# Optimization experiments

Measured on AMD Instinct MI355X. Metric: run time of the kernel, lower is better.

Reference implementation:

```python
import jax, jax.numpy as jnp
import numpy as np

B, P, ENC = 64, 196, 512
E, H, A, V, L = 1024, 1024, 512, 20000, 25


def setup_inputs() -> dict:
    key = jax.random.key(0)
    ks = jax.random.split(key, 20)
    s = 0.02
    return {
        "encoder_out": jax.random.normal(ks[0], (B, P, ENC), jnp.float32),
        "captions": jax.random.randint(ks[1], (B, L), 0, V),
        "lengths": L,
        # attention MLP
        "W_enc_att": jax.random.normal(ks[2], (ENC, A), jnp.float32) * s,
        "b_enc_att": jnp.zeros((A,), jnp.float32),
        "W_dec_att": jax.random.normal(ks[3], (H, A), jnp.float32) * s,
        "b_dec_att": jnp.zeros((A,), jnp.float32),
        "W_full_att": jax.random.normal(ks[4], (A, 1), jnp.float32) * s,
        "b_full_att": jnp.zeros((1,), jnp.float32),
        # embedding
        "emb_table": jax.random.normal(ks[5], (V, E), jnp.float32) * s,
        # LSTMCell: input = embedding + context -> (E+ENC, 4H)
        "W_ih": jax.random.normal(ks[6], (E + ENC, 4 * H), jnp.float32) * s,
        "b_ih": jnp.zeros((4 * H,), jnp.float32),
        "W_hh": jax.random.normal(ks[7], (H, 4 * H), jnp.float32) * s,
        "b_hh": jnp.zeros((4 * H,), jnp.float32),
        # init states
        "W_init_h": jax.random.normal(ks[8], (ENC, H), jnp.float32) * s,
        "b_init_h": jnp.zeros((H,), jnp.float32),
        "W_init_c": jax.random.normal(ks[9], (ENC, H), jnp.float32) * s,
        "b_init_c": jnp.zeros((H,), jnp.float32),
        # gate + output proj
        "W_fbeta": jax.random.normal(ks[10], (H, ENC), jnp.float32) * s,
        "b_fbeta": jnp.zeros((ENC,), jnp.float32),
        "W_fc": jax.random.normal(ks[11], (H, V), jnp.float32) * s,
        "b_fc": jnp.zeros((V,), jnp.float32),
    }


def _decode(encoder_out, W_enc_att, b_enc_att, W_dec_att, b_dec_att,
            W_full_att, b_full_att, emb_table, W_ih, b_ih, W_hh, b_hh,
            W_init_h, b_init_h, W_init_c, b_init_c, W_fbeta, b_fbeta,
            W_fc, b_fc, captions, T):
    # precompute encoder-side attention projection (constant across timesteps)
    att_enc = encoder_out @ W_enc_att + b_enc_att          # (B, P, A)
    mean_feat = encoder_out.mean(axis=1)                   # (B, ENC)
    h0 = mean_feat @ W_init_h + b_init_h
    c0 = mean_feat @ W_init_c + b_init_c
    embeddings = emb_table[captions[:, :T]]                # (B, T, E)
    xs = jnp.swapaxes(embeddings, 0, 1)                    # (T, B, E)

    def step(carry, emb_t):
        h, c = carry
        att_dec = h @ W_dec_att + b_dec_att                # (B, A)
        energy = (jax.nn.relu(att_enc + att_dec[:, None, :]) @ W_full_att
                  + b_full_att)[..., 0]                    # (B, P)
        alpha = jax.nn.softmax(energy, axis=1)
        context = jnp.einsum('bp,bpe->be', alpha, encoder_out)
        gate = jax.nn.sigmoid(h @ W_fbeta + b_fbeta)       # (B, ENC)
        x = jnp.concatenate([emb_t, gate * context], axis=1)
        gates = x @ W_ih + b_ih + h @ W_hh + b_hh          # (B, 4H)
        i, f, g, o = jnp.split(gates, 4, axis=1)           # torch order i,f,g,o
        c = jax.nn.sigmoid(f) * c + jax.nn.sigmoid(i) * jnp.tanh(g)
        h = jax.nn.sigmoid(o) * jnp.tanh(c)
        preds = h @ W_fc + b_fc                            # dropout = identity (eval)
        return (h, c), (preds, alpha)

    _, (preds, alphas) = jax.lax.scan(step, (h0, c0), xs)
    predictions = jnp.swapaxes(preds, 0, 1)                # (B, T, V)
    alphas = jnp.swapaxes(alphas, 0, 1)                    # (B, T, P)
    return predictions, alphas


def reference(encoder_out, captions, lengths, W_enc_att, b_enc_att, W_dec_att,
              b_dec_att, W_full_att, b_full_att, emb_table, W_ih, b_ih, W_hh,
              b_hh, W_init_h, b_init_h, W_init_c, b_init_c, W_fbeta, b_fbeta,
              W_fc, b_fc):
    T = int(lengths) - 1
    return _decode(encoder_out, W_enc_att, b_enc_att, W_dec_att, b_dec_att,
                   W_full_att, b_full_att, emb_table, W_ih, b_ih, W_hh, b_hh,
                   W_init_h, b_init_h, W_init_c, b_init_c, W_fbeta, b_fbeta,
                   W_fc, b_fc, captions, T)
```

## Files before the change

### kernel.cpp

```cpp
#include <hip/hip_runtime.h>
#include <hip/hip_bf16.h>

#define BB 64
#define PP 196
#define ENCD 512
#define ED 1024
#define HD 1024
#define AD 512
#define VD 20000
#define TT 24
#define VPAD 20096
#define HOFF 32768
#define NSA 4

typedef __attribute__((ext_vector_type(8))) short short8;
typedef __attribute__((ext_vector_type(4))) short short4v;
typedef __attribute__((ext_vector_type(4))) float f32x4;
typedef __attribute__((ext_vector_type(8))) _Float16 h16x8;

__device__ __forceinline__ float sigf(float x) { return 1.f / (1.f + __expf(-x)); }

__device__ __forceinline__ unsigned short f2bf(float f) {
    unsigned u = __builtin_bit_cast(unsigned, f);
    u = (u + 0x7FFFu + ((u >> 16) & 1u)) >> 16;
    return (unsigned short)u;
}
__device__ __forceinline__ void split2(float v, unsigned short& h, unsigned short& l) {
    h = f2bf(v);
    float hf = __builtin_bit_cast(float, ((unsigned)h) << 16);
    l = f2bf(v - hf);
}
__device__ __forceinline__ void split2h(float v, _Float16& h, _Float16& l) {
    h = (_Float16)v;
    l = (_Float16)(v - (float)h);
}
__device__ __forceinline__ float bf2f(unsigned short u) {
    return __builtin_bit_cast(float, ((unsigned)u) << 16);
}

__device__ __forceinline__ void split_store(
    const float* __restrict__ W, unsigned short* __restrict__ oh,
    unsigned short* __restrict__ ol, int N, int Npad, int coff,
    int rowoff, int perm, int kc, int n) {
    int src = perm ? ((n & 3) * 1024 + (n >> 2)) : n;
    short8 vh, vl;
    #pragma unroll
    for (int j = 0; j < 8; ++j) {
        float v = (src < N) ? W[(size_t)(rowoff + kc * 8 + j) * N + src] : 0.f;
        unsigned short h, l; split2(v, h, l);
        vh[j] = (short)h; vl[j] = (short)l;
    }
    size_t o = ((size_t)kc * Npad + coff + n) * 8;
    *(short8*)(oh + o) = vh; *(short8*)(ol + o) = vl;
}

__global__ __launch_bounds__(256) void megasplit_kernel(
    const float* __restrict__ W_enc, unsigned short* __restrict__ wenc_h, unsigned short* __restrict__ wenc_l,
    const float* __restrict__ W_dec, const float* __restrict__ W_fbeta, const float* __restrict__ W_hh,
    unsigned short* __restrict__ wbig_h, unsigned short* __restrict__ wbig_l,
    const float* __restrict__ W_ih,
    unsigned short* __restrict__ wih1_h, unsigned short* __restrict__ wih1_l,
    unsigned short* __restrict__ wih2_h, unsigned short* __restrict__ wih2_l,
    const float* __restrict__ b_ih, const float* __restrict__ b_hh, float* __restrict__ biasp,
    const int* __restrict__ captions, const float* __restrict__ table,
    unsigned short* __restrict__ embc_h, unsigned short* __restrict__ embc_l) {
    int bid = blockIdx.x, tid = threadIdx.x;
    if (bid < 128) {
        int local = bid, xb = local & 1, kc = local >> 1;
        split_store(W_enc, wenc_h, wenc_l, 512, 512, 0, 0, 0, kc, xb * 256 + tid);
    } else if (bid < 384) {
        int local = bid - 128, xb = local & 1, kc = local >> 1;
        split_store(W_dec, wbig_h, wbig_l, 512, 5120, 0, 0, 0, kc, xb * 256 + tid);
    } else if (bid < 640) {
        int local = bid - 384, xb = local & 1, kc = local >> 1;
        split_store(W_fbeta, wbig_h, wbig_l, 512, 5120, 512, 0, 0, kc, xb * 256 + tid);
    } else if (bid < 2688) {
        int local = bid - 640, xb = local & 15, kc = local >> 4;
        split_store(W_hh, wbig_h, wbig_l, 4096, 5120, 1024, 0, 1, kc, xb * 256 + tid);
    } else if (bid < 4736) {
        int local = bid - 2688, xb = local & 15, kc = local >> 4;
        split_store(W_ih, wih1_h, wih1_l, 4096, 4096, 0, 0, 1, kc, xb * 256 + tid);
    } else if (bid < 5760) {
        int local = bid - 4736, xb = local & 15, kc = local >> 4;
        split_store(W_ih, wih2_h, wih2_l, 4096, 4096, 0, 1024, 1, kc, xb * 256 + tid);
    } else if (bid < 5776) {
        int n = (bid - 5760) * 256 + tid;
        int src = (n & 3) * 1024 + (n >> 2);
        biasp[n] = b_ih[src] + b_hh[src];
    } else {
        int local = bid - 5776;
        int t = local >> 6, b = local & 63;
        if (tid < 128) {
            int kc = tid;
            int tok = captions[b * 25 + t];
            const float* row = table + (size_t)tok * ED + kc * 8;
            short8 vh, vl;
            #pragma unroll
            for (int j = 0; j < 8; ++j) {
                unsigned short h, l; split2(row[j], h, l);
                vh[j] = (short)h; vl[j] = (short)l;
            }
            size_t o = ((size_t)kc * (TT * BB) + t * BB + b) * 8;
            *(short8*)(embc_h + o) = vh; *(short8*)(embc_l + o) = vl;
        }
    }
}

__global__ __launch_bounds__(256) void enc2bf16_kernel(
    const float* __restrict__ enc, unsigned short* __restrict__ encb) {
    size_t idx = ((size_t)blockIdx.x * 256 + threadIdx.x) * 8;
    float4 v0 = *(const float4*)(enc + idx);
    float4 v1 = *(const float4*)(enc + idx + 4);
    short8 o;
    o[0] = (short)f2bf(v0.x); o[1] = (short)f2bf(v0.y);
    o[2] = (short)f2bf(v0.z); o[3] = (short)f2bf(v0.w);
    o[4] = (short)f2bf(v1.x); o[5] = (short)f2bf(v1.y);
    o[6] = (short)f2bf(v1.z); o[7] = (short)f2bf(v1.w);
    *(short8*)(encb + idx) = o;
}

__global__ __launch_bounds__(256) void split_w_fp16_kernel(
    const float* __restrict__ W, _Float16* __restrict__ oq,
    int N, int Npad, int Nlaunch) {
    int n = blockIdx.x * 256 + threadIdx.x;
    if (n >= Nlaunch) return;
    int kc = blockIdx.y;
    h16x8 v;
    #pragma unroll
    for (int j = 0; j < 8; ++j)
        v[j] = (_Float16)((n < N) ? W[(size_t)(kc * 8 + j) * N + n] : 0.f);
    *(h16x8*)(oq + ((size_t)kc * Npad + n) * 8) = v;
}

__global__ __launch_bounds__(512) void mean_kernel(const float* __restrict__ enc,
                                                   float* __restrict__ mf) {
    int b = blockIdx.x; int e = threadIdx.x;
    const float* base = enc + (size_t)b * PP * ENCD + e;
    float s = 0.f;
    #pragma unroll 4
    for (int p = 0; p < PP; ++p) s += base[(size_t)p * ENCD];
    mf[b * ENCD + e] = s * (1.f / PP);
}

__global__ __launch_bounds__(256) void init_hc_kernel(
    const float* __restrict__ mf,
    const float* __restrict__ Wh, const float* __restrict__ bh,
    const float* __restrict__ Wc, const float* __restrict__ bc,
    unsigned short* __restrict__ hc_h, unsigned short* __restrict__ hc_l,
    float* __restrict__ c0) {
    int b = blockIdx.x;
    int isC = blockIdx.y;
    const float* W    = isC ? Wc : Wh;
    const float* bias = isC ? bc : bh;
    __shared__ float smf[ENCD];
    for (int i = threadIdx.x; i < ENCD; i += 256) smf[i] = mf[b * ENCD + i];
    __syncthreads();
    #pragma unroll
    for (int jj = 0; jj < 4; ++jj) {
        int j = threadIdx.x + jj * 256;
        float acc = bias[j];
        for (int k = 0; k < ENCD; ++k) acc += smf[k] * W[(size_t)k * HD + j];
        if (isC) c0[b * HD + j] = acc;
        else {
            unsigned short h, l; split2(acc, h, l);
            size_t o = ((size_t)(j >> 3) * 64 + b) * 8 + (j & 7);
            hc_h[o] = h; hc_l[o] = l;
        }
    }
}

__global__ __launch_bounds__(256) void mfma_gemm_bigf(
    const float* __restrict__ Ap,
    const unsigned short* __restrict__ Bh, const unsigned short* __restrict__ Bl,
    const float* __restrict__ bias, float* __restrict__ C,
    int N, int Npad, int K, int Mtiles, int Ntiles, int inner_m, int half_out) {
    __shared__ __align__(16) short lds[32768];
    short* Ahs = lds;
    short* Als = lds + 8192;
    short* Bhs = lds + 16384;
    short* Bls = lds + 24576;
    int tid = threadIdx.x, lane = tid & 63, w = tid >> 6;
    int nwg = Mtiles * Ntiles;
    int orig = blockIdx.x;
    int q = nwg >> 3, r = nwg & 7;
    int xcd = orig & 7;
    int basew = (xcd < r) ? xcd * (q + 1) : r * (q + 1) + (xcd - r) * q;
    int wg = basew + (orig >> 3);
    int mt, nt;
    if (inner_m) { mt = wg % Mtiles; nt = wg / Mtiles; }
    else         { nt = wg % Ntiles; mt = wg / Ntiles; }
    int m0 = mt * 128, n0 = nt * 128;
    int wr = w >> 1, wc = w & 1;
    f32x4 acc[4][4];
    #pragma unroll
    for (int i = 0; i < 4; ++i)
        #pragma unroll
        for (int j = 0; j < 4; ++j) acc[i][j] = (f32x4){0.f, 0.f, 0.f, 0.f};
    int nsteps = K >> 6;
    float4 va[8];
    short8 rb[2][4];
    auto load_step = [&](int s) {
        int k0 = s * 64, kc0 = s * 8;
        #pragma unroll
        for (int it = 0; it < 8; ++it) {
            int idx = it * 256 + tid; int m = idx >> 4, k4 = idx & 15;
            va[it] = *(const float4*)(Ap + (size_t)(m0 + m) * K + k0 + k4 * 4);
        }
        #pragma unroll
        for (int it = 0; it < 4; ++it) {
            int g = w * 4 + it; int kcl = g >> 1; int rb0 = (g & 1) * 64;
            size_t gb = ((size_t)(kc0 + kcl) * Npad + n0 + rb0 + lane) * 8;
            rb[0][it] = *(const short8*)(Bh + gb);
            rb[1][it] = *(const short8*)(Bl + gb);
        }
    };
    load_step(0);
    for (int s = 0; s < nsteps; ++s) {
        __syncthreads();
        #pragma unroll
        for (int it = 0; it < 8; ++it) {
            int idx = it * 256 + tid; int m = idx >> 4, k4 = idx & 15;
            int kc = k4 >> 1, jh = (k4 & 1) * 4;
            float vv[4] = {va[it].x, va[it].y, va[it].z, va[it].w};
            short4v hv, lv;
            #pragma unroll
            for (int qq = 0; qq < 4; ++qq) {
                unsigned short h, l; split2(vv[qq], h, l);
                hv[qq] = (short)h; lv[qq] = (short)l;
            }
            int o = kc * 1024 + ((m ^ kc) << 3) + jh;
            *(short4v*)(Ahs + o) = hv;
            *(short4v*)(Als + o) = lv;
        }
        #pragma unroll
        for (int it = 0; it < 4; ++it) {
            int g = w * 4 + it; int kcl = g >> 1; int rb0 = (g & 1) * 64;
            int o = (kcl * 128 + rb0 + lane) * 8;
            *(short8*)(Bhs + o) = rb[0][it];
            *(short8*)(Bls + o) = rb[1][it];
        }
        __syncthreads();
        if (s + 1 < nsteps) load_step(s + 1);
        #pragma unroll
        for (int ks = 0; ks < 2; ++ks) {
            int kq = ks * 4 + (lane >> 4);
            short8 afh[4], afl[4], bfh[4], bfl[4];
            #pragma unroll
            for (int mi = 0; mi < 4; ++mi) {
                int row = wr * 64 + mi * 16 + (lane & 15);
                int o = kq * 1024 + ((row ^ kq) << 3);
                afh[mi] = *(const short8*)(Ahs + o);
                afl[mi] = *(const short8*)(Als + o);
            }
            #pragma unroll
            for (int ni = 0; ni < 4; ++ni) {
                int o = (kq * 128 + wc * 64 + ni * 16 + (lane & 15)) * 8;
                bfh[ni] = *(const short8*)(Bhs + o);
                bfl[ni] = *(const short8*)(Bls + o);
            }
            #pragma unroll
            for (int mi = 0; mi < 4; ++mi)
                #pragma unroll
                for (int ni = 0; ni < 4; ++ni) {
                    acc[mi][ni] = __builtin_amdgcn_mfma_f32_16x16x32_bf16(afh[mi], bfh[ni], acc[mi][ni], 0, 0, 0);
                    acc[mi][ni] = __builtin_amdgcn_mfma_f32_16x16x32_bf16(afh[mi], bfl[ni], acc[mi][ni], 0, 0, 0);
                    acc[mi][ni] = __builtin_amdgcn_mfma_f32_16x16x32_bf16(afl[mi], bfh[ni], acc[mi][ni], 0, 0, 0);
                }
        }
    }
    #pragma unroll
    for (int mi = 0; mi < 4; ++mi) {
        int rrow = m0 + wr * 64 + mi * 16 + ((lane >> 4) << 2);
        #pragma unroll
        for (int ni = 0; ni < 4; ++ni) {
            int c = n0 + wc * 64 + ni * 16 + (lane & 15);
            if (c < N) {
                float bv = bias ? bias[c] : 0.f;
                if (half_out) {
                    _Float16* Ch = (_Float16*)C;
                    #pragma unroll
                    for (int qq = 0; qq < 4; ++qq)
                        Ch[(size_t)(rrow + qq) * N + c] = (_Float16)(acc[mi][ni][qq] + bv);
                } else {
                    #pragma unroll
                    for (int qq = 0; qq < 4; ++qq)
                        C[(size_t)(rrow + qq) * N + c] = acc[mi][ni][qq] + bv;
                }
            }
        }
    }
}

__global__ __launch_bounds__(256) void mfma_gemm_bigp(
    const unsigned short* __restrict__ Ah, const unsigned short* __restrict__ Al,
    const unsigned short* __restrict__ Bh, const unsigned short* __restrict__ Bl,
    const float* __restrict__ bias, float* __restrict__ C,
    int Mtot, int N, int Npad, int K, int Mtiles, int Ntiles, int inner_m) {
    __shared__ __align__(16) short lds[32768];
    short* Ahs = lds;
    short* Als = lds + 8192;
    short* Bhs = lds + 16384;
    short* Bls = lds + 24576;
    int tid = threadIdx.x, lane = tid & 63, w = tid >> 6;
    int nwg = Mtiles * Ntiles;
    int orig = blockIdx.x;
    int q = nwg >> 3, r = nwg & 7;
    int xcd = orig & 7;
    int basew = (xcd < r) ? xcd * (q + 1) : r * (q + 1) + (xcd - r) * q;
    int wg = basew + (orig >> 3);
    int mt, nt;
    if (inner_m) { mt = wg % Mtiles; nt = wg / Mtiles; }
    else         { nt = wg % Ntiles; mt = wg / Ntiles; }
    int m0 = mt * 128, n0 = nt * 128;
    int wr = w >> 1, wc = w & 1;
    f32x4 acc[4][4];
    #pragma unroll
    for (int i = 0; i < 4; ++i)
        #pragma unroll
        for (int j = 0; j < 4; ++j) acc[i][j] = (f32x4){0.f, 0.f, 0.f, 0.f};
    int nsteps = K >> 6;
    short8 ra[2][4], rb[2][4];
    auto load_step = [&](int s) {
        int kc0 = s * 8;
        #pragma unroll
        for (int it = 0; it < 4; ++it) {
            int idx = it * 256 + tid; int kcl = idx >> 7, row = idx & 127;
            size_t ga = ((size_t)(kc0 + kcl) * Mtot + m0 + row) * 8;
            ra[0][it] = *(const short8*)(Ah + ga);
            ra[1][it] = *(const short8*)(Al + ga);
        }
        #pragma unroll
        for (int it = 0; it < 4; ++it) {
            int g = w * 4 + it; int kcl = g >> 1; int rb0 = (g & 1) * 64;
            size_t gb = ((size_t)(kc0 + kcl) * Npad + n0 + rb0 + lane) * 8;
            rb[0][it] = *(const short8*)(Bh + gb);
            rb[1][it] = *(const short8*)(Bl + gb);
        }
    };
    load_step(0);
    for (int s = 0; s < nsteps; ++s) {
        __syncthreads();
        #pragma unroll
        for (int it = 0; it < 4; ++it) {
            int idx = it * 256 + tid; int kcl = idx >> 7, row = idx & 127;
            int o = (kcl * 128 + row) * 8;
            *(short8*)(Ahs + o) = ra[0][it];
            *(short8*)(Als + o) = ra[1][it];
        }
        #pragma unroll
        for (int it = 0; it < 4; ++it) {
            int g = w * 4 + it; int kcl = g >> 1; int rb0 = (g & 1) * 64;
            int o = (kcl * 128 + rb0 + lane) * 8;
            *(short8*)(Bhs + o) = rb[0][it];
            *(short8*)(Bls + o) = rb[1][it];
        }
        __syncthreads();
        if (s + 1 < nsteps) load_step(s + 1);
        #pragma unroll
        for (int ks = 0; ks < 2; ++ks) {
            int kq = ks * 4 + (lane >> 4);
            short8 afh[4], afl[4], bfh[4], bfl[4];
            #pragma unroll
            for (int mi = 0; mi < 4; ++mi) {
                int o = (kq * 128 + wr * 64 + mi * 16 + (lane & 15)) * 8;
                afh[mi] = *(const short8*)(Ahs + o);
                afl[mi] = *(const short8*)(Als + o);
            }
            #pragma unroll
            for (int ni = 0; ni < 4; ++ni) {
                int o = (kq * 128 + wc * 64 + ni * 16 + (lane & 15)) * 8;
                bfh[ni] = *(const short8*)(Bhs + o);
                bfl[ni] = *(const short8*)(Bls + o);
            }
            #pragma unroll
            for (int mi = 0; mi < 4; ++mi)
                #pragma unroll
                for (int ni = 0; ni < 4; ++ni) {
                    acc[mi][ni] = __builtin_amdgcn_mfma_f32_16x16x32_bf16(afh[mi], bfh[ni], acc[mi][ni], 0, 0, 0);
                    acc[mi][ni] = __builtin_amdgcn_mfma_f32_16x16x32_bf16(afh[mi], bfl[ni], acc[mi][ni], 0, 0, 0);
                    acc[mi][ni] = __builtin_amdgcn_mfma_f32_16x16x32_bf16(afl[mi], bfh[ni], acc[mi][ni], 0, 0, 0);
                }
        }
    }
    #pragma unroll
    for (int mi = 0; mi < 4; ++mi) {
        int rrow = m0 + wr * 64 + mi * 16 + ((lane >> 4) << 2);
        #pragma unroll
        for (int ni = 0; ni < 4; ++ni) {
            int c = n0 + wc * 64 + ni * 16 + (lane & 15);
            if (c < N) {
                float bv = bias ? bias[c] : 0.f;
                #pragma unroll
                for (int qq = 0; qq < 4; ++qq)
                    C[(size_t)(rrow + qq) * N + c] = acc[mi][ni][qq] + bv;
            }
        }
    }
}

__global__ __launch_bounds__(256) void mfma_gemm_fp16(
    const _Float16* __restrict__ Ah, const _Float16* __restrict__ Al,
    const _Float16* __restrict__ Bq,
    const float* __restrict__ bias, float* __restrict__ C,
    int Mtot, int N, int Npad, int K, int Mtiles, int Ntiles) {
    __shared__ __align__(16) _Float16 lds[24576];
    _Float16* Ahs = lds;
    _Float16* Als = lds + 8192;
    _Float16* Bs  = lds + 16384;
    int tid = threadIdx.x, lane = tid & 63, w = tid >> 6;
    int nwg = Mtiles * Ntiles;
    int orig = blockIdx.x;
    int q = nwg >> 3, r = nwg & 7;
    int xcd = orig & 7;
    int basew = (xcd < r) ? xcd * (q + 1) : r * (q + 1) + (xcd - r) * q;
    int wg = basew + (orig >> 3);
    int mt = wg % Mtiles, nt = wg / Mtiles;
    int m0 = mt * 128, n0 = nt * 128;
    int wr = w >> 1, wc = w & 1;
    f32x4 acc[4][4];
    #pragma unroll
    for (int i = 0; i < 4; ++i)
        #pragma unroll
        for (int j = 0; j < 4; ++j) acc[i][j] = (f32x4){0.f, 0.f, 0.f, 0.f};
    int nsteps = K >> 6;
    h16x8 ra[2][4], rb[4];
    auto load_step = [&](int s) {
        int kc0 = s * 8;
        #pragma unroll
        for (int it = 0; it < 4; ++it) {
            int idx = it * 256 + tid; int kcl = idx >> 7, row = idx & 127;
            size_t ga = ((size_t)(kc0 + kcl) * Mtot + m0 + row) * 8;
            ra[0][it] = *(const h16x8*)(Ah + ga);
            ra[1][it] = *(const h16x8*)(Al + ga);
        }
        #pragma unroll
        for (int it = 0; it < 4; ++it) {
            int idx = it * 256 + tid; int kcl = idx >> 7, row = idx & 127;
            size_t gb = ((size_t)(kc0 + kcl) * Npad + n0 + row) * 8;
            rb[it] = *(const h16x8*)(Bq + gb);
        }
    };
    load_step(0);
    for (int s = 0; s < nsteps; ++s) {
        __syncthreads();
        #pragma unroll
        for (int it = 0; it < 4; ++it) {
            int idx = it * 256 + tid; int kcl = idx >> 7, row = idx & 127;
            int o = (kcl * 128 + row) * 8;
            *(h16x8*)(Ahs + o) = ra[0][it];
            *(h16x8*)(Als + o) = ra[1][it];
            *(h16x8*)(Bs + o)  = rb[it];
        }
        __syncthreads();
        if (s + 1 < nsteps) load_step(s + 1);
        #pragma unroll
        for (int ks = 0; ks < 2; ++ks) {
            int kq = ks * 4 + (lane >> 4);
            h16x8 afh[4], afl[4], bf[4];
            #pragma unroll
            for (int mi = 0; mi < 4; ++mi) {
                int o = (kq * 128 + wr * 64 + mi * 16 + (lane & 15)) * 8;
                afh[mi] = *(const h16x8*)(Ahs + o);
                afl[mi] = *(const h16x8*)(Als + o);
            }
            #pragma unroll
            for (int ni = 0; ni < 4; ++ni) {
                int o = (kq * 128 + wc * 64 + ni * 16 + (lane & 15)) * 8;
                bf[ni] = *(const h16x8*)(Bs + o);
            }
            #pragma unroll
            for (int mi = 0; mi < 4; ++mi)
                #pragma unroll
                for (int ni = 0; ni < 4; ++ni) {
                    acc[mi][ni] = __builtin_amdgcn_mfma_f32_16x16x32_f16(afh[mi], bf[ni], acc[mi][ni], 0, 0, 0);
                    acc[mi][ni] = __builtin_amdgcn_mfma_f32_16x16x32_f16(afl[mi], bf[ni], acc[mi][ni], 0, 0, 0);
                }
        }
    }
    #pragma unroll
    for (int mi = 0; mi < 4; ++mi) {
        int rrow = m0 + wr * 64 + mi * 16 + ((lane >> 4) << 2);
        #pragma unroll
        for (int ni = 0; ni < 4; ++ni) {
            int c = n0 + wc * 64 + ni * 16 + (lane & 15);
            if (c < N) {
                float bv = bias ? bias[c] : 0.f;
                #pragma unroll
                for (int qq = 0; qq < 4; ++qq)
                    C[(size_t)(rrow + qq) * N + c] = acc[mi][ni][qq] + bv;
            }
        }
    }
}

__global__ __launch_bounds__(256) void hgemm_direct(
    const unsigned short* __restrict__ Ah, const unsigned short* __restrict__ Al,
    const unsigned short* __restrict__ Bh, const unsigned short* __restrict__ Bl,
    float* __restrict__ out) {
    int tid = threadIdx.x, lane = tid & 63, w = tid >> 6;
    int n0 = blockIdx.x * 128 + w * 32;
    int kc0 = blockIdx.y * 32;
    out += (size_t)blockIdx.y * 64 * 5120;
    f32x4 acc[4][2];
    #pragma unroll
    for (int i = 0; i < 4; ++i)
        #pragma unroll
        for (int j = 0; j < 2; ++j) acc[i][j] = (f32x4){0.f, 0.f, 0.f, 0.f};
    #pragma unroll
    for (int s = 0; s < 8; ++s) {
        int kc = kc0 + s * 4 + (lane >> 4);
        short8 afh[4], afl[4], bfh[2], bfl[2];
        #pragma unroll
        for (int mi = 0; mi < 4; ++mi) {
            size_t o = ((size_t)kc * 64 + mi * 16 + (lane & 15)) * 8;
            afh[mi] = *(const short8*)(Ah + o);
            afl[mi] = *(const short8*)(Al + o);
        }
        #pragma unroll
        for (int ni = 0; ni < 2; ++ni) {
            size_t o = ((size_t)kc * 5120 + n0 + ni * 16 + (lane & 15)) * 8;
            bfh[ni] = *(const short8*)(Bh + o);
            bfl[ni] = *(const short8*)(Bl + o);
        }
        #pragma unroll
        for (int mi = 0; mi < 4; ++mi)
            #pragma unroll
            for (int ni = 0; ni < 2; ++ni) {
                acc[mi][ni] = __builtin_amdgcn_mfma_f32_16x16x32_bf16(afh[mi], bfh[ni], acc[mi][ni], 0, 0, 0);
                acc[mi][ni] = __builtin_amdgcn_mfma_f32_16x16x32_bf16(afh[mi], bfl[ni], acc[mi][ni], 0, 0, 0);
                acc[mi][ni] = __builtin_amdgcn_mfma_f32_16x16x32_bf16(afl[mi], bfh[ni], acc[mi][ni], 0, 0, 0);
            }
    }
    #pragma unroll
    for (int mi = 0; mi < 4; ++mi) {
        int rrow = mi * 16 + ((lane >> 4) << 2);
        #pragma unroll
        for (int ni = 0; ni < 2; ++ni) {
            int c = n0 + ni * 16 + (lane & 15);
            #pragma unroll
            for (int qq = 0; qq < 4; ++qq)
                out[(size_t)(rrow + qq) * 5120 + c] = acc[mi][ni][qq];
        }
    }
}

__global__ __launch_bounds__(1024) void attn_ctx_kernel(
    const _Float16* __restrict__ att_enc, const float* __restrict__ adg,
    const float* __restrict__ b_dec, const float* __restrict__ Wfull,
    const unsigned short* __restrict__ encb, const float* __restrict__ b_fbeta,
    float* __restrict__ alpha_out, unsigned short* __restrict__ x2h,
    unsigned short* __restrict__ x2l, int t) {
    int b = blockIdx.x; int tid = threadIdx.x;
    __shared__ float sdec[AD], sw[AD], sgate[AD], sal[256], sE[256], red[256];
    __shared__ float sctx[2][AD];
    if (tid < AD) {
        float s = b_dec[tid];
        #pragma unroll
        for (int ks = 0; ks < NSA; ++ks) s += adg[((size_t)ks * BB + b) * 5120 + tid];
        sdec[tid] = s;
        sw[tid] = Wfull[tid];
    } else {
        int e = tid - AD;
        float s = b_fbeta[e];
        #pragma unroll
        for (int ks = 0; ks < NSA; ++ks) s += adg[((size_t)ks * BB + b) * 5120 + 512 + e];
        sgate[e] = s;
    }
    __syncthreads();
    int w = tid >> 6, lane = tid & 63;
    float4 sd0 = *(const float4*)&sdec[lane * 8];
    float4 sd1 = *(const float4*)&sdec[lane * 8 + 4];
    float4 sw0 = *(const float4*)&sw[lane * 8];
    float4 sw1 = *(const float4*)&sw[lane * 8 + 4];
    for (int p = w; p < PP; p += 16) {
        const _Float16* row = att_enc + ((size_t)b * PP + p) * AD + lane * 8;
        h16x8 hv = *(const h16x8*)row;
        float part = fmaxf((float)hv[0] + sd0.x, 0.f) * sw0.x +
                     fmaxf((float)hv[1] + sd0.y, 0.f) * sw0.y +
                     fmaxf((float)hv[2] + sd0.z, 0.f) * sw0.z +
                     fmaxf((float)hv[3] + sd0.w, 0.f) * sw0.w +
                     fmaxf((float)hv[4] + sd1.x, 0.f) * sw1.x +
                     fmaxf((float)hv[5] + sd1.y, 0.f) * sw1.y +
                     fmaxf((float)hv[6] + sd1.z, 0.f) * sw1.z +
                     fmaxf((float)hv[7] + sd1.w, 0.f) * sw1.w;
        #pragma unroll
        for (int off = 32; off > 0; off >>= 1) part += __shfl_down(part, off, 64);
        if (lane == 0) sE[p] = part;
    }
    __syncthreads();
    float myE = (tid < PP) ? sE[tid] : -1e30f;
    if (tid < 256) red[tid] = myE;
    __syncthreads();
    for (int s = 128; s > 0; s >>= 1) {
        if (tid < s) red[tid] = fmaxf(red[tid], red[tid + s]);
        __syncthreads();
    }
    float mx = red[0];
    __syncthreads();
    float ex = (tid < PP) ? __expf(myE - mx) : 0.f;
    if (tid < 256) red[tid] = ex;
    __syncthreads();
    for (int s = 128; s > 0; s >>= 1) {
        if (tid < s) red[tid] += red[tid + s];
        __syncthreads();
    }
    if (tid < PP) {
        float al = ex * (1.f / red[0]);
        sal[tid] = al;
        alpha_out[((size_t)b * TT + t) * PP + tid] = al;
    }
    __syncthreads();
    int e = tid & 511, half = tid >> 9;
    const unsigned short* basep = encb + (size_t)b * PP * ENCD + e;
    float s2 = 0.f;
    #pragma unroll 2
    for (int p = half * 98; p < half * 98 + 98; ++p)
        s2 += sal[p] * bf2f(basep[(size_t)p * ENCD]);
    sctx[half][e] = s2;
    __syncthreads();
    if (tid < AD) {
        float ctx = sctx[0][tid] + sctx[1][tid];
        float gate = sigf(sgate[tid]);
        unsigned short h, l; split2(gate * ctx, h, l);
        size_t o = ((size_t)(tid >> 3) * 64 + b) * 8 + (tid & 7);
        x2h[o] = h; x2l[o] = l;
    }
}

__global__ __launch_bounds__(256) void gates_lstm2(
    const unsigned short* __restrict__ Ah, const unsigned short* __restrict__ Al,
    const unsigned short* __restrict__ Bh, const unsigned short* __restrict__ Bl,
    const float* __restrict__ pregates, const float* __restrict__ adg,
    float* __restrict__ c, unsigned short* __restrict__ ho_h,
    unsigned short* __restrict__ ho_l, _Float16* __restrict__ hfc_h,
    _Float16* __restrict__ hfc_l, int t) {
    __shared__ float gl[4][64][33];
    int tid = threadIdx.x, lane = tid & 63, w = tid >> 6;
    int n0 = blockIdx.x * 32;
    f32x4 acc[4][2];
    #pragma unroll
    for (int i = 0; i < 4; ++i)
        #pragma unroll
        for (int j = 0; j < 2; ++j) acc[i][j] = (f32x4){0.f, 0.f, 0.f, 0.f};
    #pragma unroll
    for (int s = 0; s < 4; ++s) {
        int kc = w * 16 + s * 4 + (lane >> 4);
        short8 afh[4], afl[4], bfh[2], bfl[2];
        #pragma unroll
        for (int mi = 0; mi < 4; ++mi) {
            size_t o = ((size_t)kc * 64 + mi * 16 + (lane & 15)) * 8;
            afh[mi] = *(const short8*)(Ah + o);
            afl[mi] = *(const short8*)(Al + o);
        }
        #pragma unroll
        for (int ni = 0; ni < 2; ++ni) {
            size_t o = ((size_t)kc * 4096 + n0 + ni * 16 + (lane & 15)) * 8;
            bfh[ni] = *(const short8*)(Bh + o);
            bfl[ni] = *(const short8*)(Bl + o);
        }
        #pragma unroll
        for (int mi = 0; mi < 4; ++mi)
            #pragma unroll
            for (int ni = 0; ni < 2; ++ni) {
                acc[mi][ni] = __builtin_amdgcn_mfma_f32_16x16x32_bf16(afh[mi], bfh[ni], acc[mi][ni], 0, 0, 0);
                acc[mi][ni] = __builtin_amdgcn_mfma_f32_16x16x32_bf16(afh[mi], bfl[ni], acc[mi][ni], 0, 0, 0);
                acc[mi][ni] = __builtin_amdgcn_mfma_f32_16x16x32_bf16(afl[mi], bfh[ni], acc[mi][ni], 0, 0, 0);
            }
    }
    #pragma unroll
    for (int mi = 0; mi < 4; ++mi) {
        int rrow = mi * 16 + ((lane >> 4) << 2);
        #pragma unroll
        for (int ni = 0; ni < 2; ++ni) {
            int cl = ni * 16 + (lane & 15);
            #pragma unroll
            for (int qq = 0; qq < 4; ++qq)
                gl[w][rrow + qq][cl] = acc[mi][ni][qq];
        }
    }
    __syncthreads();
    #pragma unroll
    for (int i = 0; i < 2; ++i) {
        int idx = tid + i * 256;
        int b = idx >> 3, jl = idx & 7;
        float g4[4];
        #pragma unroll
        for (int qq = 0; qq < 4; ++qq)
            g4[qq] = gl[0][b][4 * jl + qq] + gl[1][b][4 * jl + qq] +
                     gl[2][b][4 * jl + qq] + gl[3][b][4 * jl + qq];
        {
            float4 pv = *(const float4*)&pregates[((size_t)(t * 64 + b)) * 4096 + n0 + 4 * jl];
            g4[0] += pv.x; g4[1] += pv.y; g4[2] += pv.z; g4[3] += pv.w;
        }
        #pragma unroll
        for (int ks = 0; ks < NSA; ++ks) {
            float4 av = *(const float4*)&adg[((size_t)ks * BB + b) * 5120 + 1024 + n0 + 4 * jl];
            g4[0] += av.x; g4[1] += av.y; g4[2] += av.z; g4[3] += av.w;
        }
        int j = (n0 >> 2) + jl;
        float cn = sigf(g4[1]) * c[b * HD + j] + sigf(g4[0]) * tanhf(g4[2]);
        c[b * HD + j] = cn;
        float hn = sigf(g4[3]) * tanhf(cn);
        unsigned short h, l; split2(hn, h, l);
        size_t o1 = ((size_t)(j >> 3) * 64 + b) * 8 + (j & 7);
        ho_h[o1] = h; ho_l[o1] = l;
        _Float16 fh, fl; split2h(hn, fh, fl);
        size_t o2 = ((size_t)(j >> 3) * (TT * BB) + b * TT + t) * 8 + (j & 7);
        hfc_h[o2] = fh; hfc_l[o2] = fl;
    }
}

extern "C" void kernel_launch(void* const* d_in, const int* in_sizes, int n_in,
                              void* d_out, int out_size, void* d_ws, size_t ws_size,
                              hipStream_t stream) {
    const float* enc      = (const float*)d_in[0];
    const int*   captions = (const int*)d_in[1];
    const float* W_enc    = (const float*)d_in[3];
    const float* b_enc    = (const float*)d_in[4];
    const float* W_dec    = (const float*)d_in[5];
    const float* b_dec    = (const float*)d_in[6];
    const float* W_full   = (const float*)d_in[7];
    const float* table    = (const float*)d_in[9];
    const float* W_ih     = (const float*)d_in[10];
    const float* b_ih     = (const float*)d_in[11];
    const float* W_hh     = (const float*)d_in[12];
    const float* b_hh     = (const float*)d_in[13];
    const float* W_init_h = (const float*)d_in[14];
    const float* b_init_h = (const float*)d_in[15];
    const float* W_init_c = (const float*)d_in[16];
    const float* b_init_c = (const float*)d_in[17];
    const float* W_fbeta  = (const float*)d_in[18];
    const float* b_fbeta  = (const float*)d_in[19];
    const float* W_fc     = (const float*)d_in[20];
    const float* b_fc     = (const float*)d_in[21];

    float* preds  = (float*)d_out;
    float* alphas = (float*)d_out + (size_t)BB * TT * VD;

    char* base = (char*)d_ws;
    size_t off = 0;
    auto take = [&](size_t b) { void* r = (void*)(base + off); off += (b + 255) & ~(size_t)255; return r; };
    _Float16* att_enc = (_Float16*)take((size_t)12544 * 512 * 2);
    unsigned short* wbig_h = (unsigned short*)take((size_t)128 * 5120 * 8 * 2);
    unsigned short* wbig_l = (unsigned short*)take((size_t)128 * 5120 * 8 * 2);
    unsigned short* wih1_h = (unsigned short*)take((size_t)128 * 4096 * 8 * 2);
    unsigned short* wih1_l = (unsigned short*)take((size_t)128 * 4096 * 8 * 2);
    unsigned short* encb   = (unsigned short*)wih1_h;
    unsigned short* wih2_h = (unsigned short*)take((size_t)64 * 4096 * 8 * 2);
    unsigned short* wih2_l = (unsigned short*)take((size_t)64 * 4096 * 8 * 2);
    unsigned short* wenc_h = (unsigned short*)take((size_t)64 * 512 * 8 * 2);
    unsigned short* wenc_l = (unsigned short*)take((size_t)64 * 512 * 8 * 2);
    float* pregates = (float*)take((size_t)TT * BB * 4096 * 4);
    float* scratch0 = (float*)take((size_t)TT * BB * ED * 4);
    unsigned short* embc_h = (unsigned short*)scratch0;
    unsigned short* embc_l = embc_h + (size_t)128 * TT * BB * 8;
    float* adg      = scratch0;
    float* biasp    = (float*)take((size_t)4096 * 4);
    _Float16* wfc_q = (_Float16*)(base);
    float* c_buf = (float*)take((size_t)BB * HD * 4);
    float* mf    = (float*)take((size_t)BB * ENCD * 4);
    unsigned short* axh_h0 = (unsigned short*)take((size_t)192 * 64 * 8 * 2);
    unsigned short* axh_l0 = (unsigned short*)take((size_t)192 * 64 * 8 * 2);
    unsigned short* axh_h1 = (unsigned short*)take((size_t)192 * 64 * 8 * 2);
    unsigned short* axh_l1 = (unsigned short*)take((size_t)192 * 64 * 8 * 2);
    _Float16* hfc_h  = (_Float16*)take((size_t)128 * TT * BB * 8 * 2);
    _Float16* hfc_l  = (_Float16*)take((size_t)128 * TT * BB * 8 * 2);

    megasplit_kernel<<<7312, 256, 0, stream>>>(
        W_enc, wenc_h, wenc_l, W_dec, W_fbeta, W_hh, wbig_h, wbig_l,
        W_ih, wih1_h, wih1_l, wih2_h, wih2_l,
        b_ih, b_hh, biasp, captions, table, embc_h, embc_l);
    mean_kernel<<<BB, 512, 0, stream>>>(enc, mf);
    init_hc_kernel<<<dim3(BB, 2), 256, 0, stream>>>(mf, W_init_h, b_init_h, W_init_c, b_init_c,
                                                    axh_h0 + HOFF, axh_l0 + HOFF, c_buf);
    mfma_gemm_bigf<<<392, 256, 0, stream>>>(enc, wenc_h, wenc_l, b_enc, (float*)att_enc,
                                            512, 512, 512, 98, 4, 0, 1);
    mfma_gemm_bigp<<<384, 256, 0, stream>>>(embc_h, embc_l, wih1_h, wih1_l, biasp, pregates,
                                            TT * BB, 4096, 4096, 1024, 12, 32, 1);
    enc2bf16_kernel<<<3136, 256, 0, stream>>>(enc, encb);

    {
        unsigned short* ah[2] = {axh_h0, axh_h1};
        unsigned short* al[2] = {axh_l0, axh_l1};
        for (int t = 0; t < TT; ++t) {
            int par = t & 1;
            hgemm_direct<<<dim3(40, NSA), 256, 0, stream>>>(
                ah[par] + HOFF, al[par] + HOFF, wbig_h, wbig_l, adg);
            attn_ctx_kernel<<<BB, 1024, 0, stream>>>(att_enc, adg, b_dec, W_full, encb,
                                                     b_fbeta, alphas, ah[par], al[par], t);
            gates_lstm2<<<128, 256, 0, stream>>>(
                ah[par], al[par], wih2_h, wih2_l, pregates, adg, c_buf,
                ah[1 - par] + HOFF, al[1 - par] + HOFF, hfc_h, hfc_l, t);
        }
    }

    split_w_fp16_kernel<<<dim3(79, 128), 256, 0, stream>>>(W_fc, wfc_q, VD, VPAD, VPAD);
    mfma_gemm_fp16<<<1884, 256, 0, stream>>>(hfc_h, hfc_l, wfc_q, b_fc, preds,
                                             TT * BB, VD, VPAD, 1024, 12, 157);
}
```

Baseline: 1.471 ms.

## Fuse decoder attention projection into attention kernel and W_hh into gates GEMM

Removes the per-step split-bf16 MFMA GEMM over W_dec/W_fbeta/W_hh. The attention kernel now computes the decoder projection and f_beta gate itself, using a scalar fp32 dot product per block against a concatenated 1024x1024 weight. The W_hh term moves into the gates GEMM by lengthening its K dimension from 512 to 1536. This drops one kernel launch per timestep and the adg round trip. In exchange, each of the 64 attention blocks re-reads the full 4MB fp32 weight matrix with scalar FMAs, and the gates kernel does three times more K work in only 128 blocks.

```diff
diff --git a/kernel.cpp b/kernel.cpp
--- a/kernel.cpp
+++ b/kernel.cpp
@@ -11,7 +11,6 @@
 #define TT 24
 #define VPAD 20096
 #define HOFF 32768
-#define NSA 4
 
 typedef __attribute__((ext_vector_type(8))) short short8;
 typedef __attribute__((ext_vector_type(4))) short short4v;
@@ -56,11 +55,10 @@
 
 __global__ __launch_bounds__(256) void megasplit_kernel(
     const float* __restrict__ W_enc, unsigned short* __restrict__ wenc_h, unsigned short* __restrict__ wenc_l,
-    const float* __restrict__ W_dec, const float* __restrict__ W_fbeta, const float* __restrict__ W_hh,
-    unsigned short* __restrict__ wbig_h, unsigned short* __restrict__ wbig_l,
-    const float* __restrict__ W_ih,
+    const float* __restrict__ W_dec, const float* __restrict__ W_fbeta, float* __restrict__ wdecfb,
+    const float* __restrict__ W_ih, const float* __restrict__ W_hh,
     unsigned short* __restrict__ wih1_h, unsigned short* __restrict__ wih1_l,
-    unsigned short* __restrict__ wih2_h, unsigned short* __restrict__ wih2_l,
+    unsigned short* __restrict__ wg2_h, unsigned short* __restrict__ wg2_l,
     const float* __restrict__ b_ih, const float* __restrict__ b_hh, float* __restrict__ biasp,
     const int* __restrict__ captions, const float* __restrict__ table,
     unsigned short* __restrict__ embc_h, unsigned short* __restrict__ embc_l) {
@@ -68,27 +66,26 @@
     if (bid < 128) {
         int local = bid, xb = local & 1, kc = local >> 1;
         split_store(W_enc, wenc_h, wenc_l, 512, 512, 0, 0, 0, kc, xb * 256 + tid);
-    } else if (bid < 384) {
-        int local = bid - 128, xb = local & 1, kc = local >> 1;
-        split_store(W_dec, wbig_h, wbig_l, 512, 5120, 0, 0, 0, kc, xb * 256 + tid);
-    } else if (bid < 640) {
-        int local = bid - 384, xb = local & 1, kc = local >> 1;
-        split_store(W_fbeta, wbig_h, wbig_l, 512, 5120, 512, 0, 0, kc, xb * 256 + tid);
-    } else if (bid < 2688) {
-        int local = bid - 640, xb = local & 15, kc = local >> 4;
-        split_store(W_hh, wbig_h, wbig_l, 4096, 5120, 1024, 0, 1, kc, xb * 256 + tid);
-    } else if (bid < 4736) {
-        int local = bid - 2688, xb = local & 15, kc = local >> 4;
+    } else if (bid < 4224) {
+        int idx = (bid - 128) * 256 + tid;
+        int k = idx >> 10, n = idx & 1023;
+        wdecfb[idx] = (n < 512) ? W_dec[(size_t)k * 512 + n] : W_fbeta[(size_t)k * 512 + (n - 512)];
+    } else if (bid < 6272) {
+        int local = bid - 4224, xb = local & 15, kc = local >> 4;
         split_store(W_ih, wih1_h, wih1_l, 4096, 4096, 0, 0, 1, kc, xb * 256 + tid);
-    } else if (bid < 5760) {
-        int local = bid - 4736, xb = local & 15, kc = local >> 4;
-        split_store(W_ih, wih2_h, wih2_l, 4096, 4096, 0, 1024, 1, kc, xb * 256 + tid);
-    } else if (bid < 5776) {
-        int n = (bid - 5760) * 256 + tid;
+    } else if (bid < 7296) {
+        int local = bid - 6272, xb = local & 15, kc = local >> 4;
+        split_store(W_ih, wg2_h, wg2_l, 4096, 4096, 0, 1024, 1, kc, xb * 256 + tid);
+    } else if (bid < 9344) {
+        int local = bid - 7296, xb = local & 15, kc = local >> 4;
+        split_store(W_hh, wg2_h + (size_t)64 * 4096 * 8, wg2_l + (size_t)64 * 4096 * 8,
+                    4096, 4096, 0, 0, 1, kc, xb * 256 + tid);
+    } else if (bid < 9360) {
+        int n = (bid - 9344) * 256 + tid;
         int src = (n & 3) * 1024 + (n >> 2);
         biasp[n] = b_ih[src] + b_hh[src];
     } else {
-        int local = bid - 5776;
+        int local = bid - 9360;
         int t = local >> 6, b = local & 63;
         if (tid < 128) {
             int kc = tid;
@@ -493,78 +490,39 @@
     }
 }
 
-__global__ __launch_bounds__(256) void hgemm_direct(
-    const unsigned short* __restrict__ Ah, const unsigned short* __restrict__ Al,
-    const unsigned short* __restrict__ Bh, const unsigned short* __restrict__ Bl,
-    float* __restrict__ out) {
-    int tid = threadIdx.x, lane = tid & 63, w = tid >> 6;
-    int n0 = blockIdx.x * 128 + w * 32;
-    int kc0 = blockIdx.y * 32;
-    out += (size_t)blockIdx.y * 64 * 5120;
-    f32x4 acc[4][2];
-    #pragma unroll
-    for (int i = 0; i < 4; ++i)
-        #pragma unroll
-        for (int j = 0; j < 2; ++j) acc[i][j] = (f32x4){0.f, 0.f, 0.f, 0.f};
-    #pragma unroll
-    for (int s = 0; s < 8; ++s) {
-        int kc = kc0 + s * 4 + (lane >> 4);
-        short8 afh[4], afl[4], bfh[2], bfl[2];
-        #pragma unroll
-        for (int mi = 0; mi < 4; ++mi) {
-            size_t o = ((size_t)kc * 64 + mi * 16 + (lane & 15)) * 8;
-            afh[mi] = *(const short8*)(Ah + o);
-            afl[mi] = *(const short8*)(Al + o);
-        }
-        #pragma unroll
-        for (int ni = 0; ni < 2; ++ni) {
-            size_t o = ((size_t)kc * 5120 + n0 + ni * 16 + (lane & 15)) * 8;
-            bfh[ni] = *(const short8*)(Bh + o);
-            bfl[ni] = *(const short8*)(Bl + o);
-        }
-        #pragma unroll
-        for (int mi = 0; mi < 4; ++mi)
-            #pragma unroll
-            for (int ni = 0; ni < 2; ++ni) {
-                acc[mi][ni] = __builtin_amdgcn_mfma_f32_16x16x32_bf16(afh[mi], bfh[ni], acc[mi][ni], 0, 0, 0);
-                acc[mi][ni] = __builtin_amdgcn_mfma_f32_16x16x32_bf16(afh[mi], bfl[ni], acc[mi][ni], 0, 0, 0);
-                acc[mi][ni] = __builtin_amdgcn_mfma_f32_16x16x32_bf16(afl[mi], bfh[ni], acc[mi][ni], 0, 0, 0);
-            }
-    }
-    #pragma unroll
-    for (int mi = 0; mi < 4; ++mi) {
-        int rrow = mi * 16 + ((lane >> 4) << 2);
-        #pragma unroll
-        for (int ni = 0; ni < 2; ++ni) {
-            int c = n0 + ni * 16 + (lane & 15);
-            #pragma unroll
-            for (int qq = 0; qq < 4; ++qq)
-                out[(size_t)(rrow + qq) * 5120 + c] = acc[mi][ni][qq];
-        }
-    }
-}
-
-__global__ __launch_bounds__(1024) void attn_ctx_kernel(
-    const _Float16* __restrict__ att_enc, const float* __restrict__ adg,
-    const float* __restrict__ b_dec, const float* __restrict__ Wfull,
-    const unsigned short* __restrict__ encb, const float* __restrict__ b_fbeta,
+__global__ __launch_bounds__(1024) void attn2_kernel(
+    const unsigned short* __restrict__ hh, const unsigned short* __restrict__ hl,
+    const float* __restrict__ wdecfb, const float* __restrict__ b_dec,
+    const float* __restrict__ b_fbeta, const float* __restrict__ Wfull,
+    const _Float16* __restrict__ att_enc, const unsigned short* __restrict__ encb,
     float* __restrict__ alpha_out, unsigned short* __restrict__ x2h,
     unsigned short* __restrict__ x2l, int t) {
     int b = blockIdx.x; int tid = threadIdx.x;
-    __shared__ float sdec[AD], sw[AD], sgate[AD], sal[256], sE[256], red[256];
+    __shared__ float shh[1024], sdec[AD], sgate[AD], sw[AD], sal[256], sE[256], red[256];
     __shared__ float sctx[2][AD];
-    if (tid < AD) {
-        float s = b_dec[tid];
-        #pragma unroll
-        for (int ks = 0; ks < NSA; ++ks) s += adg[((size_t)ks * BB + b) * 5120 + tid];
-        sdec[tid] = s;
-        sw[tid] = Wfull[tid];
-    } else {
-        int e = tid - AD;
-        float s = b_fbeta[e];
-        #pragma unroll
-        for (int ks = 0; ks < NSA; ++ks) s += adg[((size_t)ks * BB + b) * 5120 + 512 + e];
-        sgate[e] = s;
+    if (tid < 128) {
+        short8 vh = *(const short8*)(hh + ((size_t)tid * 64 + b) * 8);
+        short8 vl = *(const short8*)(hl + ((size_t)tid * 64 + b) * 8);
+        #pragma unroll
+        for (int j = 0; j < 8; ++j)
+            shh[tid * 8 + j] = bf2f((unsigned short)vh[j]) + bf2f((unsigned short)vl[j]);
+    }
+    if (tid < AD) sw[tid] = Wfull[tid];
+    __syncthreads();
+    {
+        int n = tid;
+        float a0 = 0.f, a1 = 0.f, a2 = 0.f, a3 = 0.f;
+        const float* wp = wdecfb + n;
+        #pragma unroll 4
+        for (int k = 0; k < 1024; k += 4) {
+            a0 += shh[k]     * wp[(size_t)k * 1024];
+            a1 += shh[k + 1] * wp[(size_t)(k + 1) * 1024];
+            a2 += shh[k + 2] * wp[(size_t)(k + 2) * 1024];
+            a3 += shh[k + 3] * wp[(size_t)(k + 3) * 1024];
+        }
+        float acc = (a0 + a1) + (a2 + a3);
+        if (n < AD) sdec[n] = acc + b_dec[n];
+        else        sgate[n - AD] = acc + b_fbeta[n - AD];
     }
     __syncthreads();
     int w = tid >> 6, lane = tid & 63;
@@ -627,13 +585,12 @@
     }
 }
 
-__global__ __launch_bounds__(256) void gates_lstm2(
+__global__ __launch_bounds__(256) void gates2_kernel(
     const unsigned short* __restrict__ Ah, const unsigned short* __restrict__ Al,
     const unsigned short* __restrict__ Bh, const unsigned short* __restrict__ Bl,
-    const float* __restrict__ pregates, const float* __restrict__ adg,
-    float* __restrict__ c, unsigned short* __restrict__ ho_h,
-    unsigned short* __restrict__ ho_l, _Float16* __restrict__ hfc_h,
-    _Float16* __restrict__ hfc_l, int t) {
+    const float* __restrict__ pregates, float* __restrict__ c,
+    unsigned short* __restrict__ ho_h, unsigned short* __restrict__ ho_l,
+    _Float16* __restrict__ hfc_h, _Float16* __restrict__ hfc_l, int t) {
     __shared__ float gl[4][64][33];
     int tid = threadIdx.x, lane = tid & 63, w = tid >> 6;
     int n0 = blockIdx.x * 32;
@@ -643,8 +600,8 @@
         #pragma unroll
         for (int j = 0; j < 2; ++j) acc[i][j] = (f32x4){0.f, 0.f, 0.f, 0.f};
     #pragma unroll
-    for (int s = 0; s < 4; ++s) {
-        int kc = w * 16 + s * 4 + (lane >> 4);
+    for (int s = 0; s < 12; ++s) {
+        int kc = w * 48 + s * 4 + (lane >> 4);
         short8 afh[4], afl[4], bfh[2], bfl[2];
         #pragma unroll
         for (int mi = 0; mi < 4; ++mi) {
@@ -691,11 +648,6 @@
         {
             float4 pv = *(const float4*)&pregates[((size_t)(t * 64 + b)) * 4096 + n0 + 4 * jl];
             g4[0] += pv.x; g4[1] += pv.y; g4[2] += pv.z; g4[3] += pv.w;
-        }
-        #pragma unroll
-        for (int ks = 0; ks < NSA; ++ks) {
-            float4 av = *(const float4*)&adg[((size_t)ks * BB + b) * 5120 + 1024 + n0 + 4 * jl];
-            g4[0] += av.x; g4[1] += av.y; g4[2] += av.z; g4[3] += av.w;
         }
         int j = (n0 >> 2) + jl;
         float cn = sigf(g4[1]) * c[b * HD + j] + sigf(g4[0]) * tanhf(g4[2]);
@@ -741,20 +693,17 @@
     size_t off = 0;
     auto take = [&](size_t b) { void* r = (void*)(base + off); off += (b + 255) & ~(size_t)255; return r; };
     _Float16* att_enc = (_Float16*)take((size_t)12544 * 512 * 2);
-    unsigned short* wbig_h = (unsigned short*)take((size_t)128 * 5120 * 8 * 2);
-    unsigned short* wbig_l = (unsigned short*)take((size_t)128 * 5120 * 8 * 2);
+    unsigned short* wg2_h  = (unsigned short*)take((size_t)192 * 4096 * 8 * 2);
+    unsigned short* wg2_l  = (unsigned short*)take((size_t)192 * 4096 * 8 * 2);
     unsigned short* wih1_h = (unsigned short*)take((size_t)128 * 4096 * 8 * 2);
     unsigned short* wih1_l = (unsigned short*)take((size_t)128 * 4096 * 8 * 2);
     unsigned short* encb   = (unsigned short*)wih1_h;
-    unsigned short* wih2_h = (unsigned short*)take((size_t)64 * 4096 * 8 * 2);
-    unsigned short* wih2_l = (unsigned short*)take((size_t)64 * 4096 * 8 * 2);
+    float* wdecfb = (float*)take((size_t)1024 * 1024 * 4);
     unsigned short* wenc_h = (unsigned short*)take((size_t)64 * 512 * 8 * 2);
     unsigned short* wenc_l = (unsigned short*)take((size_t)64 * 512 * 8 * 2);
     float* pregates = (float*)take((size_t)TT * BB * 4096 * 4);
-    float* scratch0 = (float*)take((size_t)TT * BB * ED * 4);
-    unsigned short* embc_h = (unsigned short*)scratch0;
-    unsigned short* embc_l = embc_h + (size_t)128 * TT * BB * 8;
-    float* adg      = scratch0;
+    unsigned short* embc_h = (unsigned short*)take((size_t)128 * TT * BB * 8 * 2);
+    unsigned short* embc_l = (unsigned short*)take((size_t)128 * TT * BB * 8 * 2);
     float* biasp    = (float*)take((size_t)4096 * 4);
     _Float16* wfc_q = (_Float16*)(base);
     float* c_buf = (float*)take((size_t)BB * HD * 4);
@@ -766,10 +715,10 @@
     _Float16* hfc_h  = (_Float16*)take((size_t)128 * TT * BB * 8 * 2);
     _Float16* hfc_l  = (_Float16*)take((size_t)128 * TT * BB * 8 * 2);
 
-    megasplit_kernel<<<7312, 256, 0, stream>>>(
-        W_enc, wenc_h, wenc_l, W_dec, W_fbeta, W_hh, wbig_h, wbig_l,
-        W_ih, wih1_h, wih1_l, wih2_h, wih2_l,
-        b_ih, b_hh, biasp, captions, table, embc_h, embc_l);
+    megasplit_kernel<<<10896, 256, 0, stream>>>(
+        W_enc, wenc_h, wenc_l, W_dec, W_fbeta, wdecfb, W_ih, W_hh,
+        wih1_h, wih1_l, wg2_h, wg2_l, b_ih, b_hh, biasp,
+        captions, table, embc_h, embc_l);
     mean_kernel<<<BB, 512, 0, stream>>>(enc, mf);
     init_hc_kernel<<<dim3(BB, 2), 256, 0, stream>>>(mf, W_init_h, b_init_h, W_init_c, b_init_c,
                                                     axh_h0 + HOFF, axh_l0 + HOFF, c_buf);
@@ -784,12 +733,11 @@
         unsigned short* al[2] = {axh_l0, axh_l1};
         for (int t = 0; t < TT; ++t) {
             int par = t & 1;
-            hgemm_direct<<<dim3(40, NSA), 256, 0, stream>>>(
-                ah[par] + HOFF, al[par] + HOFF, wbig_h, wbig_l, adg);
-            attn_ctx_kernel<<<BB, 1024, 0, stream>>>(att_enc, adg, b_dec, W_full, encb,
-                                                     b_fbeta, alphas, ah[par], al[par], t);
-            gates_lstm2<<<128, 256, 0, stream>>>(
-                ah[par], al[par], wih2_h, wih2_l, pregates, adg, c_buf,
+            attn2_kernel<<<BB, 1024, 0, stream>>>(
+                ah[par] + HOFF, al[par] + HOFF, wdecfb, b_dec, b_fbeta, W_full,
+                att_enc, encb, alphas, ah[par], al[par], t);
+            gates2_kernel<<<128, 256, 0, stream>>>(
+                ah[par], al[par], wg2_h, wg2_l, pregates, c_buf,
                 ah[1 - par] + HOFF, al[1 - par] + HOFF, hfc_h, hfc_l, t);
         }
     }
```

After: 2.469 ms. +67.8%, slower.
